# Optimization experiments

Hardware: AMD Instinct MI355X
Metric: run time of the kernel (lower is better)

The kernel has to match this reference:

```python
import jax, jax.numpy as jnp
import numpy as np

# ---- static module config (matches init_kwargs) ----
N = 16384
E_DIM = 256
SHARE_N_E = 2048
SPECIFIC = [1024, 1024, 1024]
TOTAL_N_E = SHARE_N_E + sum(SPECIFIC)  # 5120
BETA = 0.25
NUM_MOD = len(SPECIFIC)
BIG = 1e7  # value written into masked-out distance entries

# prefix boundaries of the per-modality code blocks: [2048, 3072, 4096, 5120]
CODE_BOUNDS = jnp.asarray(np.cumsum([SHARE_N_E] + SPECIFIC)[:, None].squeeze(-1) if False else np.cumsum([SHARE_N_E] + SPECIFIC), dtype=jnp.int32)
# code -> modality id; shared codes get -1
CODE_MOD = jnp.searchsorted(CODE_BOUNDS, jnp.arange(TOTAL_N_E, dtype=jnp.int32), side='right') - 1  # [TOTAL_N_E]


def setup_inputs() -> dict:
    key = jax.random.key(0)
    k1, k2 = jax.random.split(key)
    x = jax.random.normal(k1, (N, E_DIM), dtype=jnp.float32)
    emb_weight = jax.random.normal(k2, (TOTAL_N_E, E_DIM), dtype=jnp.float32)  # nn.Embedding default N(0,1)
    split_index = jnp.array([0, 5120, 10240, 16384], dtype=jnp.int64)  # 3 equal modality segments
    return {"x": x, "emb_weight": emb_weight, "split_index": split_index}


def reference(x, emb_weight, split_index):
    # pairwise squared distances d[n, c] = ||x_n||^2 + ||e_c||^2 - 2 x_n . e_c
    d = (jnp.sum(x * x, axis=1, keepdims=True)
         + jnp.sum(emb_weight * emb_weight, axis=1)[None, :]
         - 2.0 * jnp.einsum('nd,cd->nc', x, emb_weight))  # [N, TOTAL_N_E]

    # token -> modality id via split boundaries (vectorized form of the Python loop)
    tok_mod = jnp.searchsorted(split_index, jnp.arange(N, dtype=split_index.dtype), side='right') - 1  # [N]
    tok_mod = tok_mod.astype(jnp.int32)
    # allowed = shared code OR code's modality matches token's modality
    allowed = (CODE_MOD[None, :] == -1) | (CODE_MOD[None, :] == tok_mod[:, None])  # [N, TOTAL_N_E]
    d = jnp.where(allowed, d, jnp.float32(BIG))

    indices = jnp.argmin(d, axis=-1)              # [N]
    x_q = jnp.take(emb_weight, indices, axis=0)   # [N, E_DIM]

    # per-modality VQ losses: codebook + beta * commitment (mse over segment)
    sg = jax.lax.stop_gradient
    se_commit = jnp.sum((sg(x_q) - x) ** 2, axis=1)   # [N]
    se_code = jnp.sum((x_q - sg(x)) ** 2, axis=1)     # [N]
    seg_commit = jax.ops.segment_sum(se_commit, tok_mod, num_segments=NUM_MOD)
    seg_code = jax.ops.segment_sum(se_code, tok_mod, num_segments=NUM_MOD)
    counts = (split_index[1:] - split_index[:-1]).astype(jnp.float32) * jnp.float32(E_DIM)
    q_losses = seg_code / counts + BETA * (seg_commit / counts)  # [NUM_MOD]

    # straight-through estimator
    x_q_ste = x + sg(x_q - x)
    return (x_q_ste, indices, d, q_losses)
```

## Files before the change

kernel.cpp:

```cpp
#include <hip/hip_runtime.h>
#include <stdint.h>

#define N_TOK    16384
#define E_DIM    256
#define N_CODE   5120
#define N_SHARED 2048
#define BIGF     1e7f

#define BM  128
#define BN  128
#define BK  32
#define LDK 40
#define NCB (N_CODE / BN)

#define IDX_OFF ((size_t)N_TOK * E_DIM)
#define D_OFF   (IDX_OFF + N_TOK)
#define QL_OFF  (D_OFF + (size_t)N_TOK * N_CODE)

typedef float f32x4 __attribute__((ext_vector_type(4)));
typedef short bf16x8 __attribute__((ext_vector_type(8)));

__device__ __forceinline__ unsigned short bf16_rn(float f) {
    unsigned u = __float_as_uint(f);
    u += 0x7FFF + ((u >> 16) & 1);
    return (unsigned short)(u >> 16);
}
__device__ __forceinline__ float bf16_to_f(unsigned short h) {
    return __uint_as_float(((unsigned)h) << 16);
}

__device__ __forceinline__ void cvt8(f32x4 a, f32x4 b, bf16x8& hi, bf16x8& lo) {
#pragma unroll
    for (int i = 0; i < 4; ++i) {
        unsigned short h = bf16_rn(a[i]);
        hi[i] = (short)h;
        lo[i] = (short)bf16_rn(a[i] - bf16_to_f(h));
    }
#pragma unroll
    for (int i = 0; i < 4; ++i) {
        unsigned short h = bf16_rn(b[i]);
        hi[4 + i] = (short)h;
        lo[4 + i] = (short)bf16_rn(b[i] - bf16_to_f(h));
    }
}

__global__ __launch_bounds__(256) void norms_kernel(const float* __restrict__ x,
                                                    const float* __restrict__ emb,
                                                    float* __restrict__ xx,
                                                    float* __restrict__ ee) {
    int wid = threadIdx.x >> 6, ln = threadIdx.x & 63;
    int row = blockIdx.x * 4 + wid;
    const float* src;
    float* dst;
    if (row < N_TOK) { src = x + (size_t)row * E_DIM; dst = xx + row; }
    else             { int r = row - N_TOK; src = emb + (size_t)r * E_DIM; dst = ee + r; }
    f32x4 v = ((const f32x4*)src)[ln];
    float s = v[0] * v[0] + v[1] * v[1] + v[2] * v[2] + v[3] * v[3];
#pragma unroll
    for (int sh = 32; sh; sh >>= 1) s += __shfl_xor(s, sh, 64);
    if (ln == 0) *dst = s;
}

__global__ __launch_bounds__(256, 2) void gemm_kernel(const float* __restrict__ x,
                                                      const float* __restrict__ emb,
                                                      const int* __restrict__ split,
                                                      const float* __restrict__ xx,
                                                      const float* __restrict__ ee,
                                                      float* __restrict__ out) {
    __shared__ short Ahi[BM * LDK], Alo[BM * LDK], Bhi[BN * LDK], Blo[BN * LDK];
    __shared__ float xxs[BM];
    __shared__ float ees[BN];
    __shared__ float redv[2][BM];
    __shared__ int   redi[2][BM];

    const int bx = blockIdx.x;
    const int by = blockIdx.y;
    const int m0 = by * BM, n0 = bx * BN;
    const int t = threadIdx.x;

    const int s1 = split[1], s2v = split[2];
    const int tmFirst = (m0 >= s1) + (m0 >= s2v);
    const int tmLast  = ((m0 + BM - 1) >= s1) + ((m0 + BM - 1) >= s2v);
    const bool rowUni = (tmFirst == tmLast);
    const int cmod = (n0 < N_SHARED) ? -1 : ((n0 - N_SHARED) >> 10);

    float* dOut = out + D_OFF;
    float* pmin = out;
    int*   pidx = (int*)(out + (size_t)N_TOK * NCB);

    if (cmod >= 0 && rowUni && cmod != tmFirst) {
        int row = t >> 1, ch = t & 1;
        f32x4* p = (f32x4*)(dOut + (size_t)(m0 + row) * N_CODE + n0 + ch * 64);
        f32x4 big = {BIGF, BIGF, BIGF, BIGF};
#pragma unroll
        for (int u = 0; u < 16; ++u) p[u] = big;
        if (t < BM) {
            pmin[(size_t)(m0 + t) * NCB + bx] = BIGF;
            pidx[(size_t)(m0 + t) * NCB + bx] = n0;
        }
        return;
    }

    const bool allAllowed = (cmod < 0) || (rowUni && cmod == tmFirst);

    if (t < BM) xxs[t] = xx[m0 + t];
    else        ees[t - BM] = ee[n0 + (t - BM)];

    f32x4 acc[4][4] = {};

    const int wid = t >> 6, lane = t & 63;
    const int quad = lane >> 4, ln16 = lane & 15;
    const int wr = (wid >> 1) * 64, wc = (wid & 1) * 64;

    const int srow = t >> 1, sch = (t & 1) * 16;
    const float* xg = x + (size_t)(m0 + srow) * E_DIM + sch;
    const float* eg = emb + (size_t)(n0 + srow) * E_DIM + sch;
    short* aHi = &Ahi[srow * LDK + sch];
    short* aLo = &Alo[srow * LDK + sch];
    short* bHi = &Bhi[srow * LDK + sch];
    short* bLo = &Blo[srow * LDK + sch];

    for (int kc = 0; kc < E_DIM / BK; ++kc) {
        __syncthreads();
        {
            const f32x4* xs = (const f32x4*)(xg + kc * BK);
            f32x4 f0 = xs[0], f1 = xs[1], f2 = xs[2], f3 = xs[3];
            bf16x8 h, l;
            cvt8(f0, f1, h, l);
            *(bf16x8*)aHi = h; *(bf16x8*)aLo = l;
            cvt8(f2, f3, h, l);
            *(bf16x8*)(aHi + 8) = h; *(bf16x8*)(aLo + 8) = l;
        }
        {
            const f32x4* es = (const f32x4*)(eg + kc * BK);
            f32x4 f0 = es[0], f1 = es[1], f2 = es[2], f3 = es[3];
            bf16x8 h, l;
            cvt8(f0, f1, h, l);
            *(bf16x8*)bHi = h; *(bf16x8*)bLo = l;
            cvt8(f2, f3, h, l);
            *(bf16x8*)(bHi + 8) = h; *(bf16x8*)(bLo + 8) = l;
        }
        __syncthreads();

        bf16x8 ah[4], al[4], bh[4], bl[4];
#pragma unroll
        for (int i = 0; i < 4; ++i) {
            ah[i] = *(const bf16x8*)&Ahi[(wr + i * 16 + ln16) * LDK + quad * 8];
            al[i] = *(const bf16x8*)&Alo[(wr + i * 16 + ln16) * LDK + quad * 8];
        }
#pragma unroll
        for (int j = 0; j < 4; ++j) {
            bh[j] = *(const bf16x8*)&Bhi[(wc + j * 16 + ln16) * LDK + quad * 8];
            bl[j] = *(const bf16x8*)&Blo[(wc + j * 16 + ln16) * LDK + quad * 8];
        }
#pragma unroll
        for (int i = 0; i < 4; ++i)
#pragma unroll
            for (int j = 0; j < 4; ++j) {
                acc[i][j] = __builtin_amdgcn_mfma_f32_16x16x32_bf16(ah[i], bh[j], acc[i][j], 0, 0, 0);
                acc[i][j] = __builtin_amdgcn_mfma_f32_16x16x32_bf16(ah[i], bl[j], acc[i][j], 0, 0, 0);
                acc[i][j] = __builtin_amdgcn_mfma_f32_16x16x32_bf16(al[i], bh[j], acc[i][j], 0, 0, 0);
                acc[i][j] = __builtin_amdgcn_mfma_f32_16x16x32_bf16(al[i], bl[j], acc[i][j], 0, 0, 0);
            }
    }

#pragma unroll
    for (int i = 0; i < 4; ++i) {
#pragma unroll
        for (int r = 0; r < 4; ++r) {
            int lm = wr + i * 16 + quad * 4 + r;
            int gm = m0 + lm;
            float xv = xxs[lm];
            int tmod = (gm >= s1) + (gm >= s2v);
            float best = 3.4e38f;
            int bidx = n0;
#pragma unroll
            for (int j = 0; j < 4; ++j) {
                int lnn = wc + j * 16 + ln16;
                int gn = n0 + lnn;
                float dv = fmaf(-2.f, acc[i][j][r], xv + ees[lnn]);
                if (!allAllowed) {
                    bool ok = (gn < N_SHARED) || (((gn - N_SHARED) >> 10) == tmod);
                    if (!ok) dv = BIGF;
                }
                dOut[(size_t)gm * N_CODE + gn] = dv;
                if (dv < best) { best = dv; bidx = gn; }
            }
#pragma unroll
            for (int s = 1; s < 16; s <<= 1) {
                float ov = __shfl_xor(best, s, 64);
                int   oi = __shfl_xor(bidx, s, 64);
                if (ov < best || (ov == best && oi < bidx)) { best = ov; bidx = oi; }
            }
            if (ln16 == 0) { redv[wid & 1][lm] = best; redi[wid & 1][lm] = bidx; }
        }
    }
    __syncthreads();
    if (t < BM) {
        float v0 = redv[0][t]; int i0 = redi[0][t];
        float v1 = redv[1][t]; int i1 = redi[1][t];
        if (v1 < v0 || (v1 == v0 && i1 < i0)) { v0 = v1; i0 = i1; }
        pmin[(size_t)(m0 + t) * NCB + bx] = v0;
        pidx[(size_t)(m0 + t) * NCB + bx] = i0;
    }
}

__global__ __launch_bounds__(256) void reduce_kernel(float* __restrict__ out) {
    int tk = blockIdx.x * 256 + threadIdx.x;
    const float* pmin = out;
    const int* pidx = (const int*)(out + (size_t)N_TOK * NCB);
    float best = pmin[(size_t)tk * NCB];
    int bi = pidx[(size_t)tk * NCB];
    for (int j = 1; j < NCB; ++j) {
        float v = pmin[(size_t)tk * NCB + j];
        int ii = pidx[(size_t)tk * NCB + j];
        if (v < best || (v == best && ii < bi)) { best = v; bi = ii; }
    }
    out[IDX_OFF + tk] = (float)bi;
}

__global__ __launch_bounds__(256) void gather_kernel(const float* __restrict__ x,
                                                     const float* __restrict__ emb,
                                                     const int* __restrict__ split,
                                                     float* __restrict__ out,
                                                     float* __restrict__ wsLoss) {
    __shared__ float ls[3];
    int t = threadIdx.x, wid = t >> 6, ln = t & 63;
    if (t < 3) ls[t] = 0.f;
    __syncthreads();
    int tok = blockIdx.x * 4 + wid;
    int idx = (int)out[IDX_OFF + tok];
    f32x4 e  = ((const f32x4*)(emb + (size_t)idx * E_DIM))[ln];
    f32x4 xv = ((const f32x4*)(x + (size_t)tok * E_DIM))[ln];
    f32x4 q;
    float s = 0.f;
#pragma unroll
    for (int c = 0; c < 4; ++c) {
        float d = e[c] - xv[c];
        q[c] = xv[c] + d;
        s = fmaf(d, d, s);
    }
    ((f32x4*)(out + (size_t)tok * E_DIM))[ln] = q;
#pragma unroll
    for (int sh = 32; sh; sh >>= 1) s += __shfl_xor(s, sh, 64);
    if (ln == 0) {
        int mod = (tok >= split[1]) + (tok >= split[2]);
        atomicAdd(&ls[mod], s);
    }
    __syncthreads();
    if (t < 3) wsLoss[blockIdx.x * 3 + t] = ls[t];
}

__global__ __launch_bounds__(256) void loss_kernel(const float* __restrict__ wsLoss,
                                                   const int* __restrict__ split,
                                                   float* __restrict__ out, int nblk) {
    __shared__ float red[256];
    float s[3] = {0.f, 0.f, 0.f};
    for (int b = threadIdx.x; b < nblk; b += 256) {
        s[0] += wsLoss[b * 3 + 0];
        s[1] += wsLoss[b * 3 + 1];
        s[2] += wsLoss[b * 3 + 2];
    }
    for (int m = 0; m < 3; ++m) {
        red[threadIdx.x] = s[m];
        __syncthreads();
        for (int st = 128; st; st >>= 1) {
            if (threadIdx.x < st) red[threadIdx.x] += red[threadIdx.x + st];
            __syncthreads();
        }
        if (threadIdx.x == 0) {
            float cnt = (float)(split[m + 1] - split[m]) * (float)E_DIM;
            float a = red[0] / cnt;
            out[QL_OFF + m] = a + 0.25f * a;
        }
        __syncthreads();
    }
}

extern "C" void kernel_launch(void* const* d_in, const int* in_sizes, int n_in,
                              void* d_out, int out_size, void* d_ws, size_t ws_size,
                              hipStream_t stream) {
    const float* x   = (const float*)d_in[0];
    const float* emb = (const float*)d_in[1];
    const int* split = (const int*)d_in[2];
    float* out = (float*)d_out;

    float* xx     = (float*)d_ws;
    float* ee     = xx + N_TOK;
    float* wsLoss = ee + N_CODE;
    int nblkGather = N_TOK / 4;

    norms_kernel<<<dim3((N_TOK + N_CODE) / 4), dim3(256), 0, stream>>>(x, emb, xx, ee);
    gemm_kernel<<<dim3(NCB, N_TOK / BM), dim3(256), 0, stream>>>(x, emb, split, xx, ee, out);
    reduce_kernel<<<dim3(N_TOK / 256), dim3(256), 0, stream>>>(out);
    gather_kernel<<<dim3(nblkGather), dim3(256), 0, stream>>>(x, emb, split, out, wsLoss);
    loss_kernel<<<dim3(1), dim3(256), 0, stream>>>(wsLoss, split, out, nblkGather);
}
```

Measured before the change: 512.1 us.

## Pre-split operands to tiled bf16 hi/lo and stream via direct global-to-LDS loads

A convert kernel now computes the norms and also writes bf16 hi/lo splits of x and the codebook into a tile-blocked workspace layout. The GEMM then loads these pre-converted tiles straight into LDS with global_load_lds, removing the repeated per-tile fp32-to-bf16 conversion and register staging. The lo*lo MFMA term is dropped, cutting matrix work by a quarter at a small precision cost that could flip near-tie argmins. The extra workspace pass adds some HBM traffic, and the new LDS layout has no padding, so bank conflicts on fragment reads are possible.

```diff
diff --git a/kernel.cpp b/kernel.cpp
--- a/kernel.cpp
+++ b/kernel.cpp
@@ -10,8 +10,9 @@
 #define BM  128
 #define BN  128
 #define BK  32
-#define LDK 40
 #define NCB (N_CODE / BN)
+#define NKC (E_DIM / BK)
+#define CHUNK (BM * BK)
 
 #define IDX_OFF ((size_t)N_TOK * E_DIM)
 #define D_OFF   (IDX_OFF + N_TOK)
@@ -19,6 +20,10 @@
 
 typedef float f32x4 __attribute__((ext_vector_type(4)));
 typedef short bf16x8 __attribute__((ext_vector_type(8)));
+typedef short s16x4 __attribute__((ext_vector_type(4)));
+
+typedef __attribute__((address_space(1))) const unsigned int g_u32;
+typedef __attribute__((address_space(3))) unsigned int lds_u32;
 
 __device__ __forceinline__ unsigned short bf16_rn(float f) {
     unsigned u = __float_as_uint(f);
@@ -29,45 +34,50 @@
     return __uint_as_float(((unsigned)h) << 16);
 }
 
-__device__ __forceinline__ void cvt8(f32x4 a, f32x4 b, bf16x8& hi, bf16x8& lo) {
-#pragma unroll
-    for (int i = 0; i < 4; ++i) {
-        unsigned short h = bf16_rn(a[i]);
-        hi[i] = (short)h;
-        lo[i] = (short)bf16_rn(a[i] - bf16_to_f(h));
-    }
-#pragma unroll
-    for (int i = 0; i < 4; ++i) {
-        unsigned short h = bf16_rn(b[i]);
-        hi[4 + i] = (short)h;
-        lo[4 + i] = (short)bf16_rn(b[i] - bf16_to_f(h));
-    }
-}
-
-__global__ __launch_bounds__(256) void norms_kernel(const float* __restrict__ x,
-                                                    const float* __restrict__ emb,
-                                                    float* __restrict__ xx,
-                                                    float* __restrict__ ee) {
+__global__ __launch_bounds__(256) void convert_kernel(const float* __restrict__ x,
+                                                      const float* __restrict__ emb,
+                                                      float* __restrict__ xx,
+                                                      float* __restrict__ ee,
+                                                      short* __restrict__ xhi, short* __restrict__ xlo,
+                                                      short* __restrict__ ehi, short* __restrict__ elo) {
     int wid = threadIdx.x >> 6, ln = threadIdx.x & 63;
     int row = blockIdx.x * 4 + wid;
-    const float* src;
-    float* dst;
-    if (row < N_TOK) { src = x + (size_t)row * E_DIM; dst = xx + row; }
-    else             { int r = row - N_TOK; src = emb + (size_t)r * E_DIM; dst = ee + r; }
+    const float* src; float* nrm; short *hiA, *loA; int rl, tb;
+    if (row < N_TOK) {
+        src = x + (size_t)row * E_DIM; nrm = xx + row;
+        tb = row >> 7; rl = row & 127; hiA = xhi; loA = xlo;
+    } else {
+        int r = row - N_TOK;
+        src = emb + (size_t)r * E_DIM; nrm = ee + r;
+        tb = r >> 7; rl = r & 127; hiA = ehi; loA = elo;
+    }
     f32x4 v = ((const f32x4*)src)[ln];
-    float s = v[0] * v[0] + v[1] * v[1] + v[2] * v[2] + v[3] * v[3];
+    float s = v[0]*v[0] + v[1]*v[1] + v[2]*v[2] + v[3]*v[3];
+    s16x4 h, l;
+#pragma unroll
+    for (int c = 0; c < 4; ++c) {
+        unsigned short hh = bf16_rn(v[c]);
+        h[c] = (short)hh;
+        l[c] = (short)bf16_rn(v[c] - bf16_to_f(hh));
+    }
+    int kc = ln >> 3, q = (ln >> 1) & 3, kl4 = (ln & 1) * 4;
+    size_t di = ((((size_t)tb * NKC + kc) * 4 + q) * BM + rl) * 8 + kl4;
+    *(s16x4*)&hiA[di] = h;
+    *(s16x4*)&loA[di] = l;
 #pragma unroll
     for (int sh = 32; sh; sh >>= 1) s += __shfl_xor(s, sh, 64);
-    if (ln == 0) *dst = s;
-}
-
-__global__ __launch_bounds__(256, 2) void gemm_kernel(const float* __restrict__ x,
-                                                      const float* __restrict__ emb,
+    if (ln == 0) *nrm = s;
+}
+
+__global__ __launch_bounds__(256, 2) void gemm_kernel(const short* __restrict__ xhi,
+                                                      const short* __restrict__ xlo,
+                                                      const short* __restrict__ ehi,
+                                                      const short* __restrict__ elo,
                                                       const int* __restrict__ split,
                                                       const float* __restrict__ xx,
                                                       const float* __restrict__ ee,
                                                       float* __restrict__ out) {
-    __shared__ short Ahi[BM * LDK], Alo[BM * LDK], Bhi[BN * LDK], Blo[BN * LDK];
+    __shared__ short Ah[CHUNK], Al[CHUNK], Bh[CHUNK], Bl[CHUNK];
     __shared__ float xxs[BM];
     __shared__ float ees[BN];
     __shared__ float redv[2][BM];
@@ -112,46 +122,37 @@
     const int quad = lane >> 4, ln16 = lane & 15;
     const int wr = (wid >> 1) * 64, wc = (wid & 1) * 64;
 
-    const int srow = t >> 1, sch = (t & 1) * 16;
-    const float* xg = x + (size_t)(m0 + srow) * E_DIM + sch;
-    const float* eg = emb + (size_t)(n0 + srow) * E_DIM + sch;
-    short* aHi = &Ahi[srow * LDK + sch];
-    short* aLo = &Alo[srow * LDK + sch];
-    short* bHi = &Bhi[srow * LDK + sch];
-    short* bLo = &Blo[srow * LDK + sch];
-
-    for (int kc = 0; kc < E_DIM / BK; ++kc) {
+    const short* aHiG = xhi + (size_t)by * NKC * CHUNK;
+    const short* aLoG = xlo + (size_t)by * NKC * CHUNK;
+    const short* bHiG = ehi + (size_t)bx * NKC * CHUNK;
+    const short* bLoG = elo + (size_t)bx * NKC * CHUNK;
+    const int tOff = t * 8;
+
+    for (int kc = 0; kc < NKC; ++kc) {
         __syncthreads();
-        {
-            const f32x4* xs = (const f32x4*)(xg + kc * BK);
-            f32x4 f0 = xs[0], f1 = xs[1], f2 = xs[2], f3 = xs[3];
-            bf16x8 h, l;
-            cvt8(f0, f1, h, l);
-            *(bf16x8*)aHi = h; *(bf16x8*)aLo = l;
-            cvt8(f2, f3, h, l);
-            *(bf16x8*)(aHi + 8) = h; *(bf16x8*)(aLo + 8) = l;
-        }
-        {
-            const f32x4* es = (const f32x4*)(eg + kc * BK);
-            f32x4 f0 = es[0], f1 = es[1], f2 = es[2], f3 = es[3];
-            bf16x8 h, l;
-            cvt8(f0, f1, h, l);
-            *(bf16x8*)bHi = h; *(bf16x8*)bLo = l;
-            cvt8(f2, f3, h, l);
-            *(bf16x8*)(bHi + 8) = h; *(bf16x8*)(bLo + 8) = l;
+        const int co = kc * CHUNK;
+#pragma unroll
+        for (int p = 0; p < 2; ++p) {
+            int o = p * 2048 + tOff;
+            __builtin_amdgcn_global_load_lds((g_u32*)(aHiG + co + o), (lds_u32*)&Ah[o], 16, 0, 0);
+            __builtin_amdgcn_global_load_lds((g_u32*)(aLoG + co + o), (lds_u32*)&Al[o], 16, 0, 0);
+            __builtin_amdgcn_global_load_lds((g_u32*)(bHiG + co + o), (lds_u32*)&Bh[o], 16, 0, 0);
+            __builtin_amdgcn_global_load_lds((g_u32*)(bLoG + co + o), (lds_u32*)&Bl[o], 16, 0, 0);
         }
         __syncthreads();
 
         bf16x8 ah[4], al[4], bh[4], bl[4];
 #pragma unroll
         for (int i = 0; i < 4; ++i) {
-            ah[i] = *(const bf16x8*)&Ahi[(wr + i * 16 + ln16) * LDK + quad * 8];
-            al[i] = *(const bf16x8*)&Alo[(wr + i * 16 + ln16) * LDK + quad * 8];
+            int a = (quad * BM + wr + i * 16 + ln16) * 8;
+            ah[i] = *(const bf16x8*)&Ah[a];
+            al[i] = *(const bf16x8*)&Al[a];
         }
 #pragma unroll
         for (int j = 0; j < 4; ++j) {
-            bh[j] = *(const bf16x8*)&Bhi[(wc + j * 16 + ln16) * LDK + quad * 8];
-            bl[j] = *(const bf16x8*)&Blo[(wc + j * 16 + ln16) * LDK + quad * 8];
+            int b = (quad * BM + wc + j * 16 + ln16) * 8;
+            bh[j] = *(const bf16x8*)&Bh[b];
+            bl[j] = *(const bf16x8*)&Bl[b];
         }
 #pragma unroll
         for (int i = 0; i < 4; ++i)
@@ -160,7 +161,6 @@
                 acc[i][j] = __builtin_amdgcn_mfma_f32_16x16x32_bf16(ah[i], bh[j], acc[i][j], 0, 0, 0);
                 acc[i][j] = __builtin_amdgcn_mfma_f32_16x16x32_bf16(ah[i], bl[j], acc[i][j], 0, 0, 0);
                 acc[i][j] = __builtin_amdgcn_mfma_f32_16x16x32_bf16(al[i], bh[j], acc[i][j], 0, 0, 0);
-                acc[i][j] = __builtin_amdgcn_mfma_f32_16x16x32_bf16(al[i], bl[j], acc[i][j], 0, 0, 0);
             }
     }
 
@@ -288,10 +288,14 @@
     float* xx     = (float*)d_ws;
     float* ee     = xx + N_TOK;
     float* wsLoss = ee + N_CODE;
+    short* xhi    = (short*)(wsLoss + 4096 * 3);
+    short* xlo    = xhi + (size_t)N_TOK * E_DIM;
+    short* ehi    = xlo + (size_t)N_TOK * E_DIM;
+    short* elo    = ehi + (size_t)N_CODE * E_DIM;
     int nblkGather = N_TOK / 4;
 
-    norms_kernel<<<dim3((N_TOK + N_CODE) / 4), dim3(256), 0, stream>>>(x, emb, xx, ee);
-    gemm_kernel<<<dim3(NCB, N_TOK / BM), dim3(256), 0, stream>>>(x, emb, split, xx, ee, out);
+    convert_kernel<<<dim3((N_TOK + N_CODE) / 4), dim3(256), 0, stream>>>(x, emb, xx, ee, xhi, xlo, ehi, elo);
+    gemm_kernel<<<dim3(NCB, N_TOK / BM), dim3(256), 0, stream>>>(xhi, xlo, ehi, elo, split, xx, ee, out);
     reduce_kernel<<<dim3(N_TOK / 256), dim3(256), 0, stream>>>(out);
     gather_kernel<<<dim3(nblkGather), dim3(256), 0, stream>>>(x, emb, split, out, wsLoss);
     loss_kernel<<<dim3(1), dim3(256), 0, stream>>>(wsLoss, split, out, nblkGather);
```

Result: faster. 488.2 us (-4.7%).
